# Kernel optimization log

Measured on AMD Instinct MI355X. Metric: run time of the kernel, lower is better.

The kernel has to match this reference:

```python
import jax, jax.numpy as jnp
import numpy as np

L, B, D, H, K = 1024, 64, 256, 256, 4  # nodes, batch, input dim, hidden dim, heap arity


def _build_tree_schedule():
    # Deterministic 4-ary heap tree: parent(i) = (i-1)//K; children 4i+1..4i+4.
    # First K//2 children are 'left', last K//2 are 'right'. Pad slots use index L
    # (a sentinel zero row). Levels are processed deepest-first (leaves -> root).
    depth = np.zeros(L, dtype=np.int64)
    for i in range(1, L):
        depth[i] = depth[(i - 1) // K] + 1
    n_levels = int(depth.max()) + 1
    levels = [np.where(depth == d)[0] for d in range(n_levels)]
    M = max(len(lv) for lv in levels)
    level_nodes = np.full((n_levels, M), L, dtype=np.int32)
    child_idx = np.full((n_levels, M, K), L, dtype=np.int32)
    for d, lv in enumerate(levels):
        level_nodes[d, : len(lv)] = lv
        for j, n in enumerate(lv):
            for c in range(K):
                cc = K * n + c + 1
                if cc < L:
                    child_idx[d, j, c] = cc
    return jnp.asarray(level_nodes), jnp.asarray(child_idx)


def setup_inputs() -> dict:
    key = jax.random.key(0)
    ks = jax.random.split(key, 9)
    level_nodes, child_idx = _build_tree_schedule()
    sD = 1.0 / np.sqrt(D).astype(np.float32)
    sH = 1.0 / np.sqrt(H).astype(np.float32)
    return {
        "inputs": jax.random.normal(ks[0], (L, B, D), jnp.float32),
        "level_nodes": level_nodes,
        "child_idx": child_idx,
        "W_gih": jax.random.normal(ks[1], (5 * H, D), jnp.float32) * sD,
        "b_gih": jax.random.normal(ks[2], (5 * H,), jnp.float32) * sD,
        "W_glh": jax.random.normal(ks[3], (5 * H, H), jnp.float32) * sH,
        "W_grh": jax.random.normal(ks[4], (5 * H, H), jnp.float32) * sH,
        "W_cih": jax.random.normal(ks[5], (H, D), jnp.float32) * sD,
        "b_cih": jax.random.normal(ks[6], (H,), jnp.float32) * sD,
        "W_clh": jax.random.normal(ks[7], (H, H), jnp.float32) * sH,
        "W_crh": jax.random.normal(ks[8], (H, H), jnp.float32) * sH,
    }


def _tree_gru(inputs, level_nodes, child_idx, W_gih, b_gih, W_glh, W_grh,
              W_cih, b_cih, W_clh, W_crh):
    Ln, Bn, Dn = inputs.shape
    Hn = W_cih.shape[0]
    # Sentinel zero row at index Ln for padded node/child slots.
    inp_p = jnp.concatenate([inputs, jnp.zeros((1, Bn, Dn), inputs.dtype)], axis=0)
    h = jnp.zeros((Bn, Ln + 1, Hn), inputs.dtype)
    n_levels = level_nodes.shape[0]
    half = K // 2
    for d in range(n_levels - 1, -1, -1):  # leaves first, root last
        nodes = level_nodes[d]             # [M]
        ch = child_idx[d]                  # [M, K]
        # gather + sum child hidden states per side
        left_h = h[:, ch[:, 0]] + h[:, ch[:, 1]]      # [B, M, H]
        right_h = h[:, ch[:, half]] + h[:, ch[:, half + 1]]
        x = jnp.transpose(inp_p[nodes], (1, 0, 2))    # [B, M, D]
        gates = jax.nn.sigmoid(x @ W_gih.T + b_gih + left_h @ W_glh.T + right_h @ W_grh.T)
        rl, rr, zl, zr, z = jnp.split(gates, 5, axis=-1)
        cell = jnp.tanh(x @ W_cih.T + b_cih + (rl * left_h) @ W_clh.T + (rr * right_h) @ W_crh.T)
        hidden = zl * left_h + zr * right_h + z * cell
        h = h.at[:, nodes].set(hidden)
        h = h.at[:, Ln].set(0.0)  # keep sentinel row zero (padded writes land here)
    hn = h[:, :Ln]  # [B, L, H]
    # original output order: nodes 1..L-1 then root (node 0)
    outputs = jnp.concatenate([hn[:, 1:], hn[:, :1]], axis=1)
    return outputs, hn[:, 0]


def reference(inputs, level_nodes, child_idx, W_gih, b_gih, W_glh, W_grh,
              W_cih, b_cih, W_clh, W_crh):
    return _tree_gru(inputs, level_nodes, child_idx, W_gih, b_gih, W_glh, W_grh,
                     W_cih, b_cih, W_clh, W_crh)
```

## Files before the change

### kernel.cpp

```cpp
#include <hip/hip_runtime.h>


#define L_TOT 1024

typedef __attribute__((ext_vector_type(8))) short short8;
typedef __attribute__((ext_vector_type(4))) short short4v;
typedef __attribute__((ext_vector_type(4))) float f32x4;

static __device__ __forceinline__ float bf2f(unsigned short u) {
  unsigned int x = ((unsigned int)u) << 16;
  return __builtin_bit_cast(float, x);
}
static __device__ __forceinline__ unsigned short f2bf(float f) {
  unsigned int u = __builtin_bit_cast(unsigned int, f);
  u += 0x7fffu + ((u >> 16) & 1u);
  return (unsigned short)(u >> 16);
}
static __device__ __forceinline__ float sigmf(float x) { return 1.0f / (1.0f + __expf(-x)); }
static __device__ __forceinline__ float tanhf_(float x) { return 2.0f / (1.0f + __expf(-2.0f * x)) - 1.0f; }

static __device__ __forceinline__ void bar_lgkm() {
  asm volatile("s_waitcnt lgkmcnt(0)" ::: "memory");
  __builtin_amdgcn_s_barrier();
  __builtin_amdgcn_sched_barrier(0);
}

static __device__ __forceinline__ int swz_t(int orig, int nwg) {
  int q = nwg >> 3, r = nwg & 7, x = orig & 7, s = orig >> 3;
  return (x < r ? x * (q + 1) : r * (q + 1) + (x - r) * q) + s;
}

__global__ __launch_bounds__(256) void k_pre(
    const float* __restrict__ in,
    const float* __restrict__ Wgih, const float* __restrict__ Wglh, const float* __restrict__ Wgrh,
    const float* __restrict__ Wcih, const float* __restrict__ Wclh, const float* __restrict__ Wcrh,
    unsigned short* __restrict__ xb, unsigned short* __restrict__ Wg,
    unsigned short* __restrict__ Wc, unsigned short* __restrict__ Wl,
    unsigned short* __restrict__ hb) {
  long long t = (long long)blockIdx.x * 256 + threadIdx.x;
  if (t < 2097152LL) {
    const float* s = in + t * 8;
    short8 v;
#pragma unroll
    for (int j = 0; j < 8; ++j) v[j] = (short)f2bf(s[j]);
    *(short8*)(xb + t * 8) = v;
  }
  const int NG = 1280 * 768;
  const int NC = 256 * 768;
  const int NL = 512 * 256;
  int ti = (int)t;
  if (ti < NG) {
    int g = ti / 768, k = ti % 768;
    float v = (k < 256) ? Wgih[g * 256 + k] : ((k < 512) ? Wglh[g * 256 + k - 256] : Wgrh[g * 256 + k - 512]);
    Wg[ti] = f2bf(v);
  } else if (ti < NG + NC) {
    int t2 = ti - NG;
    int g = t2 / 768, k = t2 % 768;
    float v = (k < 256) ? Wcih[g * 256 + k] : ((k < 512) ? Wclh[g * 256 + k - 256] : Wcrh[g * 256 + k - 512]);
    Wc[t2] = f2bf(v);
  } else if (ti < NG + NC + NL) {
    int t2 = ti - NG - NC;
    int n = t2 >> 8, k = t2 & 255;
    int g = n >> 4;
    int hc = (g >> 1) * 16 + (n & 15);
    float v = (g & 1) ? Wcih[hc * 256 + k] : Wgih[(1024 + hc) * 256 + k];
    Wl[t2] = f2bf(v);
  }
  if (ti < 16384) hb[(size_t)1024 * 16384 + ti] = 0;
  if (ti < 32768) xb[(size_t)65536 * 256 + ti] = 0;
}

__global__ __launch_bounds__(256) void k_prep(const unsigned short* __restrict__ hb,
                                              unsigned short* __restrict__ lh,
                                              unsigned short* __restrict__ rh,
                                              int rows, int row_off, int lvl_start) {
  int t = blockIdx.x * 256 + threadIdx.x;
  if (t >= rows * 32) return;
  int r = t >> 5, k8 = (t & 31) << 3;
  int gr = row_off + r;
  int node = lvl_start + (gr >> 6);
  int b = gr & 63;
  int cb = 4 * node + 1;
  int c0 = cb, c1 = cb + 1, c2 = cb + 2, c3 = cb + 3;
  c0 = (c0 < L_TOT) ? c0 : L_TOT;
  c1 = (c1 < L_TOT) ? c1 : L_TOT;
  c2 = (c2 < L_TOT) ? c2 : L_TOT;
  c3 = (c3 < L_TOT) ? c3 : L_TOT;
  const short8 v0 = *(const short8*)(hb + (size_t)c0 * 16384 + b * 256 + k8);
  const short8 v1 = *(const short8*)(hb + (size_t)c1 * 16384 + b * 256 + k8);
  const short8 v2 = *(const short8*)(hb + (size_t)c2 * 16384 + b * 256 + k8);
  const short8 v3 = *(const short8*)(hb + (size_t)c3 * 16384 + b * 256 + k8);
  short8 ol, orr;
#pragma unroll
  for (int j = 0; j < 8; ++j) {
    ol[j] = (short)f2bf(bf2f((unsigned short)v0[j]) + bf2f((unsigned short)v1[j]));
    orr[j] = (short)f2bf(bf2f((unsigned short)v2[j]) + bf2f((unsigned short)v3[j]));
  }
  *(short8*)(lh + (size_t)r * 256 + k8) = ol;
  *(short8*)(rh + (size_t)r * 256 + k8) = orr;
}

template <int EPI>
static __device__ __forceinline__ void gemm_body(
    const unsigned short* __restrict__ Aseg0,
    const unsigned short* __restrict__ Aseg1,
    const unsigned short* __restrict__ Aseg2,
    const unsigned short* __restrict__ Wt, const float* __restrict__ bias,
    const float* __restrict__ bias2,
    int rows, int row_off, int lvl_start, int NT, int nwg,
    const unsigned short* __restrict__ lh, const unsigned short* __restrict__ rh,
    unsigned short* __restrict__ a2l, unsigned short* __restrict__ a2r,
    unsigned short* __restrict__ p1, unsigned short* __restrict__ p2,
    unsigned short* __restrict__ zb, unsigned short* __restrict__ hb) {
  constexpr int NKT = (EPI == 2) ? 4 : 12;
  constexpr int WSTRIDE = (EPI == 2) ? 256 : 768;
  constexpr int LR = 72;
  int t = swz_t(blockIdx.x, nwg);
  int tm = t / NT, tn = t % NT;
  const int tid = threadIdx.x, lane = tid & 63, wave = tid >> 6;
  const int wr = wave >> 1, wcl = wave & 1;

  __shared__ unsigned short As[2][128 * LR];
  __shared__ unsigned short Bs[2][128 * LR];

  f32x4 acc[2][4];
#pragma unroll
  for (int i = 0; i < 2; ++i)
#pragma unroll
    for (int j = 0; j < 4; ++j) {
      f32x4 zv = {0.f, 0.f, 0.f, 0.f};
      acc[i][j] = zv;
    }

  const unsigned short* segs[3] = {Aseg0, Aseg1, Aseg2};
  const int srow = tid >> 3;
  const int scol = (tid & 7) * 8;

  short8 rva[2][2], rvb[2][2];

  auto LOADK = [&](int kt, int s) {
    const unsigned short* segp = segs[kt >> 2];
    int ko = (kt & 3) * 64;
#pragma unroll
    for (int i = 0; i < 2; ++i) {
      int row = srow + i * 64;
      rva[s][i] = *(const short8*)(segp + (size_t)(tm * 128 + row) * 256 + ko + scol);
      rvb[s][i] = *(const short8*)(Wt + (size_t)(tn * 128 + row) * WSTRIDE + kt * 64 + scol);
    }
  };
  auto WRITEK = [&](int s, int buf) {
#pragma unroll
    for (int i = 0; i < 2; ++i) {
      int row = srow + i * 64;
      *(short8*)(&As[buf][row * LR + scol]) = rva[s][i];
      *(short8*)(&Bs[buf][row * LR + scol]) = rvb[s][i];
    }
  };

  LOADK(0, 0);
  if (NKT > 1) LOADK(1, 1);
  WRITEK(0, 0);
  bar_lgkm();

#pragma unroll
  for (int kt = 0; kt < NKT; ++kt) {
    const int cur = kt & 1;
    if (kt + 1 < NKT) WRITEK((kt + 1) & 1, cur ^ 1);
    if (kt + 2 < NKT) LOADK(kt + 2, kt & 1);
#pragma unroll
    for (int kk = 0; kk < 2; ++kk) {
      short8 af[2], bf[4];
#pragma unroll
      for (int mf = 0; mf < 2; ++mf)
        af[mf] = *(const short8*)(&As[cur][(wr * 32 + mf * 16 + (lane & 15)) * LR + kk * 32 + (lane >> 4) * 8]);
#pragma unroll
      for (int nf = 0; nf < 4; ++nf)
        bf[nf] = *(const short8*)(&Bs[cur][(wcl * 64 + nf * 16 + (lane & 15)) * LR + kk * 32 + (lane >> 4) * 8]);
#pragma unroll
      for (int mf = 0; mf < 2; ++mf)
#pragma unroll
        for (int nf = 0; nf < 4; ++nf)
          acc[mf][nf] = __builtin_amdgcn_mfma_f32_16x16x32_bf16(bf[nf], af[mf], acc[mf][nf], 0, 0, 0);
    }
    if (kt + 1 < NKT) bar_lgkm();
  }

  if (EPI == 2) {
#pragma unroll
    for (int nfp = 0; nfp < 2; ++nfp) {
      int nz = nfp * 2;
      int g = tn * 8 + wcl * 4 + nz;
      int hcq = (g >> 1) * 16 + (lane >> 4) * 4;
      f32x4 bzv = *(const f32x4*)(bias + 1024 + hcq);
      f32x4 bcv = *(const f32x4*)(bias2 + hcq);
#pragma unroll
      for (int mf = 0; mf < 2; ++mf) {
        int r = tm * 128 + wr * 32 + mf * 16 + (lane & 15);
        int node = 256 + (r >> 6), b = r & 63;
        short4v hv;
#pragma unroll
        for (int j = 0; j < 4; ++j) {
          float h = sigmf(acc[mf][nz][j] + bzv[j]) * tanhf_(acc[mf][nz + 1][j] + bcv[j]);
          hv[j] = (short)f2bf(h);
        }
        *(short4v*)(hb + (size_t)node * 16384 + b * 256 + hcq) = hv;
      }
    }
    return;
  }
#pragma unroll
  for (int nf = 0; nf < 4; ++nf) {
    int colq = tn * 128 + wcl * 64 + nf * 16 + (lane >> 4) * 4;
    f32x4 bsv = *(const f32x4*)(bias + colq);
    if (EPI == 0) {
      int ck = colq >> 8;
      int gcq = colq & 255;
#pragma unroll
      for (int mf = 0; mf < 2; ++mf) {
        int r = tm * 128 + wr * 32 + mf * 16 + (lane & 15);
        if (r < rows) {
          size_t idx = (size_t)r * 256 + gcq;
          f32x4 s;
#pragma unroll
          for (int j = 0; j < 4; ++j) s[j] = sigmf(acc[mf][nf][j] + bsv[j]);
          short4v res;
          if (ck == 4) {
#pragma unroll
            for (int j = 0; j < 4; ++j) res[j] = (short)f2bf(s[j]);
            *(short4v*)(zb + idx) = res;
          } else {
            const unsigned short* src = (ck == 0 || ck == 2) ? lh : rh;
            short4v hv = *(const short4v*)(src + idx);
#pragma unroll
            for (int j = 0; j < 4; ++j) res[j] = (short)f2bf(s[j] * bf2f((unsigned short)hv[j]));
            if (ck == 0)      *(short4v*)(a2l + idx) = res;
            else if (ck == 1) *(short4v*)(a2r + idx) = res;
            else if (ck == 2) *(short4v*)(p1 + idx) = res;
            else              *(short4v*)(p2 + idx) = res;
          }
        }
      }
    } else {
#pragma unroll
      for (int mf = 0; mf < 2; ++mf) {
        int r = tm * 128 + wr * 32 + mf * 16 + (lane & 15);
        if (r < rows) {
          size_t idx = (size_t)r * 256 + colq;
          short4v p1v = *(const short4v*)(p1 + idx);
          short4v p2v = *(const short4v*)(p2 + idx);
          short4v zbv = *(const short4v*)(zb + idx);
          int gr = row_off + r;
          int node = lvl_start + (gr >> 6);
          int b = gr & 63;
          short4v hv;
#pragma unroll
          for (int j = 0; j < 4; ++j) {
            float cell = tanhf_(acc[mf][nf][j] + bsv[j]);
            float hid = bf2f((unsigned short)p1v[j]) + bf2f((unsigned short)p2v[j]) +
                        bf2f((unsigned short)zbv[j]) * cell;
            hv[j] = (short)f2bf(hid);
          }
          *(short4v*)(hb + (size_t)node * 16384 + b * 256 + colq) = hv;
        }
      }
    }
  }
}

__global__ __launch_bounds__(512, 4) void k_gates(
    const unsigned short* __restrict__ A0, const unsigned short* __restrict__ A1,
    const unsigned short* __restrict__ A2, const unsigned short* __restrict__ Wt,
    const float* __restrict__ bias, int rows, int row_off, int lvl_start, int nwg,
    const unsigned short* __restrict__ lh, const unsigned short* __restrict__ rh,
    unsigned short* __restrict__ a2l, unsigned short* __restrict__ a2r,
    unsigned short* __restrict__ p1, unsigned short* __restrict__ p2,
    unsigned short* __restrict__ zb) {
  gemm_body<0>(A0, A1, A2, Wt, bias, nullptr, rows, row_off, lvl_start, 10, nwg,
               lh, rh, a2l, a2r, p1, p2, zb, nullptr);
}

__global__ __launch_bounds__(512, 4) void k_cell(
    const unsigned short* __restrict__ A0, const unsigned short* __restrict__ A1,
    const unsigned short* __restrict__ A2, const unsigned short* __restrict__ Wt,
    const float* __restrict__ bias, int rows, int row_off, int lvl_start, int nwg,
    const unsigned short* __restrict__ p1, const unsigned short* __restrict__ p2,
    const unsigned short* __restrict__ zb, unsigned short* __restrict__ hb) {
  gemm_body<1>(A0, A1, A2, Wt, bias, nullptr, rows, row_off, lvl_start, 2, nwg,
               nullptr, nullptr, nullptr, nullptr, (unsigned short*)p1,
               (unsigned short*)p2, (unsigned short*)zb, hb);
}

__global__ __launch_bounds__(512, 4) void k_leaf(
    const unsigned short* __restrict__ X, const unsigned short* __restrict__ Wl,
    const float* __restrict__ bg, const float* __restrict__ bc, int nwg,
    unsigned short* __restrict__ hb) {
  gemm_body<2>(X, X, X, Wl, bg, bc, 49152, 0, 0, 4, nwg,
               nullptr, nullptr, nullptr, nullptr, nullptr, nullptr, nullptr, hb);
}

__global__ __launch_bounds__(256) void k_write_out(const unsigned short* __restrict__ hb,
                                                   float* __restrict__ out) {
  long long t = (long long)blockIdx.x * 256 + threadIdx.x;
  long long e = t * 8;
  const long long main_n = 16777216LL;
  if (e < main_n) {
    int b = (int)(e >> 18);
    int rem = (int)(e & 262143);
    int i = rem >> 8;
    int k = rem & 255;
    int node = (i + 1) & 1023;
    short8 v = *(const short8*)(hb + (size_t)node * 16384 + b * 256 + k);
    float4 o0, o1;
    o0.x = bf2f((unsigned short)v[0]); o0.y = bf2f((unsigned short)v[1]);
    o0.z = bf2f((unsigned short)v[2]); o0.w = bf2f((unsigned short)v[3]);
    o1.x = bf2f((unsigned short)v[4]); o1.y = bf2f((unsigned short)v[5]);
    o1.z = bf2f((unsigned short)v[6]); o1.w = bf2f((unsigned short)v[7]);
    *(float4*)(out + e) = o0;
    *(float4*)(out + e + 4) = o1;
  } else if (e < main_n + 16384) {
    int e2 = (int)(e - main_n);
    int b = e2 >> 8, k = e2 & 255;
    short8 v = *(const short8*)(hb + (size_t)b * 256 + k);
    float4 o0, o1;
    o0.x = bf2f((unsigned short)v[0]); o0.y = bf2f((unsigned short)v[1]);
    o0.z = bf2f((unsigned short)v[2]); o0.w = bf2f((unsigned short)v[3]);
    o1.x = bf2f((unsigned short)v[4]); o1.y = bf2f((unsigned short)v[5]);
    o1.z = bf2f((unsigned short)v[6]); o1.w = bf2f((unsigned short)v[7]);
    *(float4*)(out + e) = o0;
    *(float4*)(out + e + 4) = o1;
  }
}

extern "C" void kernel_launch(void* const* d_in, const int* in_sizes, int n_in,
                              void* d_out, int out_size, void* d_ws, size_t ws_size,
                              hipStream_t stream) {
  const float* inputs = (const float*)d_in[0];
  const float* W_gih = (const float*)d_in[3];
  const float* b_gih = (const float*)d_in[4];
  const float* W_glh = (const float*)d_in[5];
  const float* W_grh = (const float*)d_in[6];
  const float* W_cih = (const float*)d_in[7];
  const float* b_cih = (const float*)d_in[8];
  const float* W_clh = (const float*)d_in[9];
  const float* W_crh = (const float*)d_in[10];
  float* out = (float*)d_out;

  char* ws = (char*)d_ws;
  size_t cur = 0;
  auto alloc = [&](size_t bytes) -> char* {
    char* p = ws + cur;
    cur += (bytes + 255) & ~(size_t)255;
    return p;
  };

  unsigned short* xb = (unsigned short*)alloc((size_t)(65536 + 128) * 256 * 2);
  unsigned short* hb = (unsigned short*)alloc((size_t)1025 * 16384 * 2);
  unsigned short* Wg = (unsigned short*)alloc((size_t)1280 * 768 * 2);
  unsigned short* Wc = (unsigned short*)alloc((size_t)256 * 768 * 2);
  unsigned short* Wl = (unsigned short*)alloc((size_t)512 * 256 * 2);

  size_t rem = (ws_size > cur) ? (ws_size - cur) : 0;
  long long rcap = (long long)(rem / (7 * 512 + 64));
  rcap = (rcap / 128) * 128;
  int Rchunk = (int)((rcap < 11008) ? rcap : 11008);
  if (Rchunk < 128) Rchunk = 128;

  unsigned short* lh  = (unsigned short*)alloc((size_t)Rchunk * 512);
  unsigned short* rh  = (unsigned short*)alloc((size_t)Rchunk * 512);
  unsigned short* a2l = (unsigned short*)alloc((size_t)Rchunk * 512);
  unsigned short* a2r = (unsigned short*)alloc((size_t)Rchunk * 512);
  unsigned short* p1  = (unsigned short*)alloc((size_t)Rchunk * 512);
  unsigned short* p2  = (unsigned short*)alloc((size_t)Rchunk * 512);
  unsigned short* zb  = (unsigned short*)alloc((size_t)Rchunk * 512);

  k_pre<<<8192, 256, 0, stream>>>(inputs, W_gih, W_glh, W_grh, W_cih, W_clh, W_crh,
                                  xb, Wg, Wc, Wl, hb);

  k_leaf<<<1536, 512, 0, stream>>>(xb + (size_t)16384 * 256, Wl, b_gih, b_cih, 1536, hb);

  static const int LSi[5] = {0, 1, 5, 21, 85};
  static const int LCi[5] = {1, 4, 16, 64, 171};

  for (int d = 4; d >= 0; --d) {
    int rows_lvl = LCi[d] * 64;
    for (int off = 0; off < rows_lvl; off += Rchunk) {
      int rows = rows_lvl - off;
      if (rows > Rchunk) rows = Rchunk;
      int tmn = (rows + 127) / 128;
      int pgrid = (rows * 32 + 255) / 256;
      k_prep<<<pgrid, 256, 0, stream>>>(hb, lh, rh, rows, off, LSi[d]);
      const unsigned short* xseg = xb + (size_t)(LSi[d] * 64 + off) * 256;
      int nwg_g = tmn * 10;
      k_gates<<<nwg_g, 512, 0, stream>>>(xseg, lh, rh, Wg, b_gih, rows, off, LSi[d], nwg_g,
                                         lh, rh, a2l, a2r, p1, p2, zb);
      int nwg_c = tmn * 2;
      k_cell<<<nwg_c, 512, 0, stream>>>(xseg, a2l, a2r, Wc, b_cih, rows, off, LSi[d], nwg_c,
                                        p1, p2, zb, hb);
    }
  }

  k_write_out<<<8200, 256, 0, stream>>>(hb, out);
}
```

Measured before the change: 267.1 us.

## Fuse fp32-to-bf16 input conversion into leaf GEMM and deepen prefetch pipeline

Result: no change. 262.3 us (-1.8%).

```diff
diff --git a/kernel.cpp b/kernel.cpp
--- a/kernel.cpp
+++ b/kernel.cpp
@@ -37,37 +37,35 @@
     unsigned short* __restrict__ xb, unsigned short* __restrict__ Wg,
     unsigned short* __restrict__ Wc, unsigned short* __restrict__ Wl,
     unsigned short* __restrict__ hb) {
-  long long t = (long long)blockIdx.x * 256 + threadIdx.x;
-  if (t < 2097152LL) {
-    const float* s = in + t * 8;
+  int t = blockIdx.x * 256 + threadIdx.x;
+  if (t < 524288) {
+    const float* s = in + (size_t)t * 8;
     short8 v;
 #pragma unroll
     for (int j = 0; j < 8; ++j) v[j] = (short)f2bf(s[j]);
-    *(short8*)(xb + t * 8) = v;
+    *(short8*)(xb + (size_t)t * 8) = v;
   }
   const int NG = 1280 * 768;
   const int NC = 256 * 768;
   const int NL = 512 * 256;
-  int ti = (int)t;
-  if (ti < NG) {
-    int g = ti / 768, k = ti % 768;
+  if (t < NG) {
+    int g = t / 768, k = t % 768;
     float v = (k < 256) ? Wgih[g * 256 + k] : ((k < 512) ? Wglh[g * 256 + k - 256] : Wgrh[g * 256 + k - 512]);
-    Wg[ti] = f2bf(v);
-  } else if (ti < NG + NC) {
-    int t2 = ti - NG;
+    Wg[t] = f2bf(v);
+  } else if (t < NG + NC) {
+    int t2 = t - NG;
     int g = t2 / 768, k = t2 % 768;
     float v = (k < 256) ? Wcih[g * 256 + k] : ((k < 512) ? Wclh[g * 256 + k - 256] : Wcrh[g * 256 + k - 512]);
     Wc[t2] = f2bf(v);
-  } else if (ti < NG + NC + NL) {
-    int t2 = ti - NG - NC;
+  } else if (t < NG + NC + NL) {
+    int t2 = t - NG - NC;
     int n = t2 >> 8, k = t2 & 255;
     int g = n >> 4;
     int hc = (g >> 1) * 16 + (n & 15);
     float v = (g & 1) ? Wcih[hc * 256 + k] : Wgih[(1024 + hc) * 256 + k];
     Wl[t2] = f2bf(v);
   }
-  if (ti < 16384) hb[(size_t)1024 * 16384 + ti] = 0;
-  if (ti < 32768) xb[(size_t)65536 * 256 + ti] = 0;
+  if (t < 16384) hb[(size_t)1024 * 16384 + t] = 0;
 }
 
 __global__ __launch_bounds__(256) void k_prep(const unsigned short* __restrict__ hb,
@@ -102,6 +100,7 @@
 
 template <int EPI>
 static __device__ __forceinline__ void gemm_body(
+    const float* __restrict__ Af,
     const unsigned short* __restrict__ Aseg0,
     const unsigned short* __restrict__ Aseg1,
     const unsigned short* __restrict__ Aseg2,
@@ -136,15 +135,22 @@
   const int srow = tid >> 3;
   const int scol = (tid & 7) * 8;
 
-  short8 rva[2][2], rvb[2][2];
+  short8 rva[3][2], rvb[3][2];
+  f32x4 fva[3][2][2];
 
   auto LOADK = [&](int kt, int s) {
-    const unsigned short* segp = segs[kt >> 2];
     int ko = (kt & 3) * 64;
 #pragma unroll
     for (int i = 0; i < 2; ++i) {
       int row = srow + i * 64;
-      rva[s][i] = *(const short8*)(segp + (size_t)(tm * 128 + row) * 256 + ko + scol);
+      if (EPI == 2) {
+        const float* ap = Af + (size_t)(tm * 128 + row) * 256 + ko + scol;
+        fva[s][i][0] = *(const f32x4*)(ap);
+        fva[s][i][1] = *(const f32x4*)(ap + 4);
+      } else {
+        const unsigned short* segp = segs[kt >> 2];
+        rva[s][i] = *(const short8*)(segp + (size_t)(tm * 128 + row) * 256 + ko + scol);
+      }
       rvb[s][i] = *(const short8*)(Wt + (size_t)(tn * 128 + row) * WSTRIDE + kt * 64 + scol);
     }
   };
@@ -152,21 +158,32 @@
 #pragma unroll
     for (int i = 0; i < 2; ++i) {
       int row = srow + i * 64;
-      *(short8*)(&As[buf][row * LR + scol]) = rva[s][i];
+      short8 v;
+      if (EPI == 2) {
+#pragma unroll
+        for (int j = 0; j < 4; ++j) {
+          v[j] = (short)f2bf(fva[s][i][0][j]);
+          v[j + 4] = (short)f2bf(fva[s][i][1][j]);
+        }
+      } else {
+        v = rva[s][i];
+      }
+      *(short8*)(&As[buf][row * LR + scol]) = v;
       *(short8*)(&Bs[buf][row * LR + scol]) = rvb[s][i];
     }
   };
 
   LOADK(0, 0);
-  if (NKT > 1) LOADK(1, 1);
+  LOADK(1, 1);
+  if (NKT > 2) LOADK(2, 2);
   WRITEK(0, 0);
   bar_lgkm();
 
 #pragma unroll
   for (int kt = 0; kt < NKT; ++kt) {
     const int cur = kt & 1;
-    if (kt + 1 < NKT) WRITEK((kt + 1) & 1, cur ^ 1);
-    if (kt + 2 < NKT) LOADK(kt + 2, kt & 1);
+    if (kt + 1 < NKT) WRITEK((kt + 1) % 3, cur ^ 1);
+    if (kt + 3 < NKT) LOADK(kt + 3, kt % 3);
 #pragma unroll
     for (int kk = 0; kk < 2; ++kk) {
       short8 af[2], bf[4];
@@ -275,7 +292,7 @@
     unsigned short* __restrict__ a2l, unsigned short* __restrict__ a2r,
     unsigned short* __restrict__ p1, unsigned short* __restrict__ p2,
     unsigned short* __restrict__ zb) {
-  gemm_body<0>(A0, A1, A2, Wt, bias, nullptr, rows, row_off, lvl_start, 10, nwg,
+  gemm_body<0>(nullptr, A0, A1, A2, Wt, bias, nullptr, rows, row_off, lvl_start, 10, nwg,
                lh, rh, a2l, a2r, p1, p2, zb, nullptr);
 }
 
@@ -285,16 +302,16 @@
     const float* __restrict__ bias, int rows, int row_off, int lvl_start, int nwg,
     const unsigned short* __restrict__ p1, const unsigned short* __restrict__ p2,
     const unsigned short* __restrict__ zb, unsigned short* __restrict__ hb) {
-  gemm_body<1>(A0, A1, A2, Wt, bias, nullptr, rows, row_off, lvl_start, 2, nwg,
+  gemm_body<1>(nullptr, A0, A1, A2, Wt, bias, nullptr, rows, row_off, lvl_start, 2, nwg,
                nullptr, nullptr, nullptr, nullptr, (unsigned short*)p1,
                (unsigned short*)p2, (unsigned short*)zb, hb);
 }
 
 __global__ __launch_bounds__(512, 4) void k_leaf(
-    const unsigned short* __restrict__ X, const unsigned short* __restrict__ Wl,
+    const float* __restrict__ X, const unsigned short* __restrict__ Wl,
     const float* __restrict__ bg, const float* __restrict__ bc, int nwg,
     unsigned short* __restrict__ hb) {
-  gemm_body<2>(X, X, X, Wl, bg, bc, 49152, 0, 0, 4, nwg,
+  gemm_body<2>(X, nullptr, nullptr, nullptr, Wl, bg, bc, 49152, 0, 0, 4, nwg,
                nullptr, nullptr, nullptr, nullptr, nullptr, nullptr, nullptr, hb);
 }
 
@@ -353,7 +370,7 @@
     return p;
   };
 
-  unsigned short* xb = (unsigned short*)alloc((size_t)(65536 + 128) * 256 * 2);
+  unsigned short* xb = (unsigned short*)alloc((size_t)(16384 + 128) * 256 * 2);
   unsigned short* hb = (unsigned short*)alloc((size_t)1025 * 16384 * 2);
   unsigned short* Wg = (unsigned short*)alloc((size_t)1280 * 768 * 2);
   unsigned short* Wc = (unsigned short*)alloc((size_t)256 * 768 * 2);
@@ -373,10 +390,10 @@
   unsigned short* p2  = (unsigned short*)alloc((size_t)Rchunk * 512);
   unsigned short* zb  = (unsigned short*)alloc((size_t)Rchunk * 512);
 
-  k_pre<<<8192, 256, 0, stream>>>(inputs, W_gih, W_glh, W_grh, W_cih, W_clh, W_crh,
+  k_pre<<<5120, 256, 0, stream>>>(inputs, W_gih, W_glh, W_grh, W_cih, W_clh, W_crh,
                                   xb, Wg, Wc, Wl, hb);
 
-  k_leaf<<<1536, 512, 0, stream>>>(xb + (size_t)16384 * 256, Wl, b_gih, b_cih, 1536, hb);
+  k_leaf<<<1536, 512, 0, stream>>>(inputs + (size_t)16384 * 256, Wl, b_gih, b_cih, 1536, hb);
 
   static const int LSi[5] = {0, 1, 5, 21, 85};
   static const int LCi[5] = {1, 4, 16, 64, 171};
```
